# Kernel optimization log

Hardware: AMD Instinct MI355X
Metric: run time of the kernel (lower is better)

## Reference

```python
import jax, jax.numpy as jnp
import numpy as np

N_EDGES = 1_000_000  # also n_atoms (module uses h_s.shape[0] as n_atoms)
N_RADIAL = 8


def setup_inputs() -> dict:
    key = jax.random.key(0)
    k1, k2, k3, k4 = jax.random.split(key, 4)
    dn = jax.random.normal(k1, (N_EDGES, 3), dtype=jnp.float32)
    h_s = jax.random.normal(k2, (N_EDGES, N_RADIAL), dtype=jnp.float32)
    basis = jax.random.uniform(k3, (N_EDGES, N_RADIAL), dtype=jnp.float32)
    idx_i = jax.random.randint(k4, (N_EDGES,), 0, N_EDGES, dtype=jnp.int32)
    return {"dn": dn, "h_s": h_s, "basis": basis, "idx_i": idx_i}


def reference(dn, h_s, basis, idx_i):
    n_atoms = h_s.shape[0]
    # per-edge moments
    zero_moment = h_s * basis                                   # [nbrs, r]
    first_moment = zero_moment[:, :, None] * dn[:, None, :]     # [nbrs, r, 3]
    # scatter-add edges -> atoms
    zero_moment = jax.ops.segment_sum(zero_moment, idx_i, num_segments=n_atoms)   # [a, r]
    first_moment = jax.ops.segment_sum(first_moment, idx_i, num_segments=n_atoms)  # [a, r, 3]
    # contractions over the small radial/spatial dims
    h_s0 = zero_moment                                           # [a, r]
    h_s1 = jnp.einsum('ari,asi->ars', first_moment, first_moment)  # [a, r, r]
    h_s1 = h_s1.reshape(n_atoms, -1)                             # [a, r*r]
    h_p = jnp.einsum('ar,asi->airs', zero_moment, first_moment)  # [a, 3, r, r]
    h_p = h_p.reshape(n_atoms, 3, -1)                            # [a, 3, r*r]
    h_s_out = jnp.concatenate([h_s0, h_s1], axis=-1)             # [a, r + r*r]
    return h_s_out, h_p
```

## Files before the change

kernel.cpp:

```cpp
#include <hip/hip_runtime.h>

#define NR 8
#define SCAN_BS 256
#define SCAN_E  1024
#define FIN_ATOMS 128


__device__ __forceinline__ unsigned short f2b(float f) {
    unsigned int u = __float_as_uint(f);
    unsigned int r = (u + 0x7FFFu + ((u >> 16) & 1u)) >> 16;
    return (unsigned short)r;
}
__device__ __forceinline__ float b2f(unsigned short h) {
    return __uint_as_float(((unsigned int)h) << 16);
}

__global__ void count_kernel(const int* __restrict__ idx,
                             int* __restrict__ cnt,
                             int* __restrict__ rank, int n_edges) {
    int e = blockIdx.x * blockDim.x + threadIdx.x;
    if (e < n_edges) rank[e] = atomicAdd(&cnt[idx[e]], 1);
}

__global__ void scan1_kernel(const int* __restrict__ cnt,
                             int* __restrict__ scanned,
                             int* __restrict__ partial, int n) {
    __shared__ int sh[SCAN_BS];
    int b = blockIdx.x, t = threadIdx.x;
    int base = b * SCAN_E + t * 4;
    int c0 = (base + 0 < n) ? cnt[base + 0] : 0;
    int c1 = (base + 1 < n) ? cnt[base + 1] : 0;
    int c2 = (base + 2 < n) ? cnt[base + 2] : 0;
    int c3 = (base + 3 < n) ? cnt[base + 3] : 0;
    int s = c0 + c1 + c2 + c3;
    sh[t] = s;
    __syncthreads();
    for (int off = 1; off < SCAN_BS; off <<= 1) {
        int v = (t >= off) ? sh[t - off] : 0;
        __syncthreads();
        sh[t] += v;
        __syncthreads();
    }
    int incl = sh[t];
    int excl = incl - s;
    if (base + 0 < n) scanned[base + 0] = excl;
    if (base + 1 < n) scanned[base + 1] = excl + c0;
    if (base + 2 < n) scanned[base + 2] = excl + c0 + c1;
    if (base + 3 < n) scanned[base + 3] = excl + c0 + c1 + c2;
    if (t == SCAN_BS - 1) partial[b] = incl;
}

__global__ void scan2_kernel(int* __restrict__ partial, int nb) {
    __shared__ int sh[1024];
    int t = threadIdx.x;
    int v = (t < nb) ? partial[t] : 0;
    sh[t] = v;
    __syncthreads();
    for (int off = 1; off < 1024; off <<= 1) {
        int u = (t >= off) ? sh[t - off] : 0;
        __syncthreads();
        sh[t] += u;
        __syncthreads();
    }
    if (t < nb) partial[t] = sh[t] - v;
}

__global__ void scan3_kernel(int* __restrict__ offsets,
                             const int* __restrict__ partial,
                             int n, int total) {
    int i = blockIdx.x * blockDim.x + threadIdx.x;
    if (i < n) offsets[i] += partial[i >> 10];
    if (i == 0) offsets[n] = total;
}

__global__ void __launch_bounds__(256) scatter24_kernel(
        const float* __restrict__ dn,
        const float* __restrict__ hs,
        const float* __restrict__ basis,
        const int*   __restrict__ idx,
        const int*   __restrict__ offsets,
        const int*   __restrict__ rank,
        unsigned short* __restrict__ ordered,
        int n_edges) {
    int e = blockIdx.x * blockDim.x + threadIdx.x;
    if (e >= n_edges) return;

    const float4* hsp = reinterpret_cast<const float4*>(hs + (size_t)e * NR);
    const float4* bp  = reinterpret_cast<const float4*>(basis + (size_t)e * NR);
    float4 h0 = hsp[0], h1 = hsp[1];
    float4 b0 = bp[0],  b1 = bp[1];

    float d0 = dn[(size_t)e * 3 + 0];
    float d1 = dn[(size_t)e * 3 + 1];
    float d2 = dn[(size_t)e * 3 + 2];

    unsigned int w0 = (unsigned int)f2b(h0.x * b0.x) | ((unsigned int)f2b(h0.y * b0.y) << 16);
    unsigned int w1 = (unsigned int)f2b(h0.z * b0.z) | ((unsigned int)f2b(h0.w * b0.w) << 16);
    unsigned int w2 = (unsigned int)f2b(h1.x * b1.x) | ((unsigned int)f2b(h1.y * b1.y) << 16);
    unsigned int w3 = (unsigned int)f2b(h1.z * b1.z) | ((unsigned int)f2b(h1.w * b1.w) << 16);
    unsigned int w4 = (unsigned int)f2b(d0) | ((unsigned int)f2b(d1) << 16);
    unsigned int w5 = (unsigned int)f2b(d2);

    int slot = offsets[idx[e]] + rank[e];
    uint2* dst = reinterpret_cast<uint2*>(ordered + (size_t)slot * 12);
    dst[0] = make_uint2(w0, w1);
    dst[1] = make_uint2(w2, w3);
    dst[2] = make_uint2(w4, w5);
}

__global__ void __launch_bounds__(256) contract_fused_kernel(
        const unsigned short* __restrict__ ordered,
        const int* __restrict__ offsets,
        float* __restrict__ out, int n_atoms) {
    __shared__ float sa[FIN_ATOMS][36];
    __shared__ int soff[FIN_ATOMS + 1];

    int a0 = blockIdx.x * FIN_ATOMS;
    int t = threadIdx.x;

    if (t < FIN_ATOMS + 1) {
        int a = a0 + t;
        soff[t] = offsets[(a <= n_atoms) ? a : n_atoms];
    }
    __syncthreads();

    int wave = t >> 6;
    int lane = t & 63;
    int half = lane >> 5;
    int l    = lane & 31;
    int k    = l - 8;
    int s_i  = k & 7;
    int i_i  = k >> 3;
    int src1 = (l < 8) ? l : s_i;
    int src2 = 8 + ((l < 8) ? 0 : i_i);
    bool isz = (l < 8);

#pragma unroll 4
    for (int p = 0; p < FIN_ATOMS / 8; ++p) {
        int al = wave * (FIN_ATOMS / 4) + p * 2 + half;
        int atom = a0 + al;
        if (atom < n_atoms) {
            int start = soff[al];
            int end   = soff[al + 1];
            float x = 0.f;
            for (int b = start; b < end; ++b) {
                const unsigned short* rec = ordered + (size_t)b * 12;
                float v1 = b2f(rec[src1]);
                float v2 = isz ? 1.0f : b2f(rec[src2]);
                x = fmaf(v1, v2, x);
            }
            sa[al][l] = x;
        }
    }
    __syncthreads();

    {
        float4* hs_base = reinterpret_cast<float4*>(out + (size_t)a0 * 72);
        for (int F = t; F < FIN_ATOMS * 18; F += 256) {
            int al = F / 18;
            int kq = F - al * 18;
            if (a0 + al >= n_atoms) break;
            const float* z = sa[al];
            float4 v;
            if (kq < 2) {
                v = reinterpret_cast<const float4*>(z)[kq];
            } else {
                int m = 4 * (kq - 2);
                int r = m >> 3, s = m & 7;
                float  fr0 = z[8 + 0 * 8 + r];
                float  fr1 = z[8 + 1 * 8 + r];
                float  fr2 = z[8 + 2 * 8 + r];
                float4 fs0 = *reinterpret_cast<const float4*>(z + 8 + 0 * 8 + s);
                float4 fs1 = *reinterpret_cast<const float4*>(z + 8 + 1 * 8 + s);
                float4 fs2 = *reinterpret_cast<const float4*>(z + 8 + 2 * 8 + s);
                v.x = fr0 * fs0.x + fr1 * fs1.x + fr2 * fs2.x;
                v.y = fr0 * fs0.y + fr1 * fs1.y + fr2 * fs2.y;
                v.z = fr0 * fs0.z + fr1 * fs1.z + fr2 * fs2.z;
                v.w = fr0 * fs0.w + fr1 * fs1.w + fr2 * fs2.w;
            }
            hs_base[F] = v;
        }
    }
    {
        float4* hp_base = reinterpret_cast<float4*>(
            out + (size_t)n_atoms * 72 + (size_t)a0 * 192);
        for (int F = t; F < FIN_ATOMS * 48; F += 256) {
            int al = F / 48;
            int kq = F - al * 48;
            if (a0 + al >= n_atoms) break;
            const float* z = sa[al];
            int i = kq >> 4;
            int m = (4 * kq) & 63;
            int r = m >> 3, s = m & 7;
            float  zr = z[r];
            float4 fv = *reinterpret_cast<const float4*>(z + 8 + i * 8 + s);
            hp_base[F] = make_float4(zr * fv.x, zr * fv.y, zr * fv.z, zr * fv.w);
        }
    }
}


__global__ void zero_acc_kernel(float* __restrict__ out, int n_atoms) {
    int tid = blockIdx.x * blockDim.x + threadIdx.x;
    if (tid >= n_atoms * 8) return;
    int atom = tid >> 3;
    int q    = tid & 7;
    float4 z = make_float4(0.f, 0.f, 0.f, 0.f);
    if (q < 2) {
        reinterpret_cast<float4*>(out + (size_t)atom * 72)[q] = z;
    } else {
        reinterpret_cast<float4*>(out + (size_t)n_atoms * 72 + (size_t)atom * 192)[q - 2] = z;
    }
}

__global__ void scatter_atomic_kernel(const float* __restrict__ dn,
                                      const float* __restrict__ hs,
                                      const float* __restrict__ basis,
                                      const int*   __restrict__ idx,
                                      float* __restrict__ out,
                                      int n_edges, int n_atoms) {
    int e = blockIdx.x * blockDim.x + threadIdx.x;
    if (e >= n_edges) return;

    const float4* hsp = reinterpret_cast<const float4*>(hs + (size_t)e * NR);
    const float4* bp  = reinterpret_cast<const float4*>(basis + (size_t)e * NR);
    float4 h0 = hsp[0], h1 = hsp[1];
    float4 b0 = bp[0],  b1 = bp[1];

    float d0 = dn[(size_t)e * 3 + 0];
    float d1 = dn[(size_t)e * 3 + 1];
    float d2 = dn[(size_t)e * 3 + 2];

    float zm[NR];
    zm[0] = h0.x * b0.x; zm[1] = h0.y * b0.y; zm[2] = h0.z * b0.z; zm[3] = h0.w * b0.w;
    zm[4] = h1.x * b1.x; zm[5] = h1.y * b1.y; zm[6] = h1.z * b1.z; zm[7] = h1.w * b1.w;

    int a = idx[e];
    float* zp = out + (size_t)a * 72;
    float* fp = out + (size_t)n_atoms * 72 + (size_t)a * 192;

#pragma unroll
    for (int r = 0; r < NR; ++r) atomicAdd(zp + r, zm[r]);
#pragma unroll
    for (int r = 0; r < NR; ++r) {
        atomicAdd(fp + r * 3 + 0, zm[r] * d0);
        atomicAdd(fp + r * 3 + 1, zm[r] * d1);
        atomicAdd(fp + r * 3 + 2, zm[r] * d2);
    }
}

__global__ void contract_inplace_kernel(float* __restrict__ out, int n_atoms) {
    int atom = blockIdx.x * 4 + (threadIdx.x >> 6);
    if (atom >= n_atoms) return;
    int lane = threadIdx.x & 63;

    float* zrow = out + (size_t)atom * 72;
    float* prow = out + (size_t)n_atoms * 72 + (size_t)atom * 192;

    float x = 0.f;
    if (lane < 8)       x = zrow[lane];
    else if (lane < 32) x = prow[lane - 8];

    int r = lane >> 3;
    int s = lane & 7;

    float zr  = __shfl(x, r);
    float fr0 = __shfl(x, 8 + r * 3 + 0);
    float fr1 = __shfl(x, 8 + r * 3 + 1);
    float fr2 = __shfl(x, 8 + r * 3 + 2);
    float fs0 = __shfl(x, 8 + s * 3 + 0);
    float fs1 = __shfl(x, 8 + s * 3 + 1);
    float fs2 = __shfl(x, 8 + s * 3 + 2);

    float hs1 = fr0 * fs0 + fr1 * fs1 + fr2 * fs2;

    zrow[8 + lane] = hs1;
    prow[lane]       = zr * fs0;
    prow[64 + lane]  = zr * fs1;
    prow[128 + lane] = zr * fs2;
}


extern "C" void kernel_launch(void* const* d_in, const int* in_sizes, int n_in,
                              void* d_out, int out_size, void* d_ws, size_t ws_size,
                              hipStream_t stream) {
    const float* dn    = (const float*)d_in[0];
    const float* hs    = (const float*)d_in[1];
    const float* basis = (const float*)d_in[2];
    const int*   idx   = (const int*)d_in[3];
    float* out = (float*)d_out;

    int n_edges = in_sizes[0] / 3;
    int n_atoms = in_sizes[1] / NR;
    int nb1 = (n_atoms + SCAN_E - 1) / SCAN_E;

    size_t off_offs = (size_t)n_atoms * 4;
    size_t off_rank = off_offs + (size_t)(n_atoms + 1) * 4;
    size_t off_part = off_rank + (size_t)n_edges * 4;
    size_t off_ord  = (off_part + (size_t)nb1 * 4 + 255) & ~(size_t)255;
    size_t ws_needed = off_ord + (size_t)n_edges * 24;

    if (ws_size >= ws_needed && nb1 <= 1024) {
        char* ws = (char*)d_ws;
        int* cnt     = (int*)ws;
        int* offsets = (int*)(ws + off_offs);
        int* rank    = (int*)(ws + off_rank);
        int* partial = (int*)(ws + off_part);
        unsigned short* ordered = (unsigned short*)(ws + off_ord);

        hipMemsetAsync(cnt, 0, (size_t)n_atoms * 4, stream);

        int blk = 256;
        count_kernel<<<(n_edges + blk - 1) / blk, blk, 0, stream>>>(
            idx, cnt, rank, n_edges);

        scan1_kernel<<<nb1, SCAN_BS, 0, stream>>>(cnt, offsets, partial, n_atoms);
        scan2_kernel<<<1, 1024, 0, stream>>>(partial, nb1);
        scan3_kernel<<<(n_atoms + blk - 1) / blk, blk, 0, stream>>>(
            offsets, partial, n_atoms, n_edges);

        scatter24_kernel<<<(n_edges + blk - 1) / blk, blk, 0, stream>>>(
            dn, hs, basis, idx, offsets, rank, ordered, n_edges);

        contract_fused_kernel<<<(n_atoms + FIN_ATOMS - 1) / FIN_ATOMS, 256, 0, stream>>>(
            ordered, offsets, out, n_atoms);
    } else {
        int blk = 256;
        int total = n_atoms * 8;
        zero_acc_kernel<<<(total + blk - 1) / blk, blk, 0, stream>>>(out, n_atoms);
        scatter_atomic_kernel<<<(n_edges + blk - 1) / blk, blk, 0, stream>>>(
            dn, hs, basis, idx, out, n_edges, n_atoms);
        contract_inplace_kernel<<<(n_atoms + 3) / 4, 256, 0, stream>>>(out, n_atoms);
    }
}
```

Measured before the change: 346.8 us.

## Bucket edges by 128-atom block and accumulate with LDS atomics

Replaces the per-atom counting sort (per-atom counts, three-stage scan, per-edge rank) with a coarse sort into 128-atom buckets. Bucket counts are scanned in a single block, and edges are scattered through atomic cursors, with the local atom index packed into the spare 16 bits of each record. The contract kernel streams each bucket's records coalesced and accumulates the 32 moment values per edge with shared-memory float atomics. This removes the rank array, two scan launches and the serial per-atom loops, at the cost of 32 LDS atomics per edge and a nondeterministic summation order.

```diff
diff --git a/kernel.cpp b/kernel.cpp
--- a/kernel.cpp
+++ b/kernel.cpp
@@ -1,9 +1,8 @@
 #include <hip/hip_runtime.h>
 
 #define NR 8
-#define SCAN_BS 256
-#define SCAN_E  1024
 #define FIN_ATOMS 128
+#define MAX_NB 8192
 
 
 __device__ __forceinline__ unsigned short f2b(float f) {
@@ -15,71 +14,57 @@
     return __uint_as_float(((unsigned int)h) << 16);
 }
 
-__global__ void count_kernel(const int* __restrict__ idx,
-                             int* __restrict__ cnt,
-                             int* __restrict__ rank, int n_edges) {
+__global__ void count_bucket_kernel(const int* __restrict__ idx,
+                                    int* __restrict__ cnt, int n_edges) {
     int e = blockIdx.x * blockDim.x + threadIdx.x;
-    if (e < n_edges) rank[e] = atomicAdd(&cnt[idx[e]], 1);
-}
-
-__global__ void scan1_kernel(const int* __restrict__ cnt,
-                             int* __restrict__ scanned,
-                             int* __restrict__ partial, int n) {
-    __shared__ int sh[SCAN_BS];
-    int b = blockIdx.x, t = threadIdx.x;
-    int base = b * SCAN_E + t * 4;
-    int c0 = (base + 0 < n) ? cnt[base + 0] : 0;
-    int c1 = (base + 1 < n) ? cnt[base + 1] : 0;
-    int c2 = (base + 2 < n) ? cnt[base + 2] : 0;
-    int c3 = (base + 3 < n) ? cnt[base + 3] : 0;
-    int s = c0 + c1 + c2 + c3;
+    if (e < n_edges) atomicAdd(&cnt[idx[e] >> 7], 1);
+}
+
+__global__ void __launch_bounds__(1024) scan_bucket_kernel(
+        const int* __restrict__ cnt,
+        int* __restrict__ boff,
+        int* __restrict__ cursor,
+        int nb, int total) {
+    __shared__ int sh[1024];
+    int t = threadIdx.x;
+    int per = (nb + 1023) >> 10;
+    int base = t * per;
+    int loc[8];
+    int s = 0;
+#pragma unroll 8
+    for (int k = 0; k < 8; ++k) {
+        if (k < per) {
+            int v = (base + k < nb) ? cnt[base + k] : 0;
+            loc[k] = s;
+            s += v;
+        }
+    }
     sh[t] = s;
     __syncthreads();
-    for (int off = 1; off < SCAN_BS; off <<= 1) {
+    for (int off = 1; off < 1024; off <<= 1) {
         int v = (t >= off) ? sh[t - off] : 0;
         __syncthreads();
         sh[t] += v;
         __syncthreads();
     }
-    int incl = sh[t];
-    int excl = incl - s;
-    if (base + 0 < n) scanned[base + 0] = excl;
-    if (base + 1 < n) scanned[base + 1] = excl + c0;
-    if (base + 2 < n) scanned[base + 2] = excl + c0 + c1;
-    if (base + 3 < n) scanned[base + 3] = excl + c0 + c1 + c2;
-    if (t == SCAN_BS - 1) partial[b] = incl;
-}
-
-__global__ void scan2_kernel(int* __restrict__ partial, int nb) {
-    __shared__ int sh[1024];
-    int t = threadIdx.x;
-    int v = (t < nb) ? partial[t] : 0;
-    sh[t] = v;
-    __syncthreads();
-    for (int off = 1; off < 1024; off <<= 1) {
-        int u = (t >= off) ? sh[t - off] : 0;
-        __syncthreads();
-        sh[t] += u;
-        __syncthreads();
-    }
-    if (t < nb) partial[t] = sh[t] - v;
-}
-
-__global__ void scan3_kernel(int* __restrict__ offsets,
-                             const int* __restrict__ partial,
-                             int n, int total) {
-    int i = blockIdx.x * blockDim.x + threadIdx.x;
-    if (i < n) offsets[i] += partial[i >> 10];
-    if (i == 0) offsets[n] = total;
-}
-
-__global__ void __launch_bounds__(256) scatter24_kernel(
+    int excl = sh[t] - s;
+#pragma unroll 8
+    for (int k = 0; k < 8; ++k) {
+        if (k < per && base + k < nb) {
+            int o = excl + loc[k];
+            boff[base + k]   = o;
+            cursor[base + k] = o;
+        }
+    }
+    if (t == 0) boff[nb] = total;
+}
+
+__global__ void __launch_bounds__(256) scatter_bucket_kernel(
         const float* __restrict__ dn,
         const float* __restrict__ hs,
         const float* __restrict__ basis,
         const int*   __restrict__ idx,
-        const int*   __restrict__ offsets,
-        const int*   __restrict__ rank,
+        int*         __restrict__ cursor,
         unsigned short* __restrict__ ordered,
         int n_edges) {
     int e = blockIdx.x * blockDim.x + threadIdx.x;
@@ -93,64 +78,69 @@
     float d0 = dn[(size_t)e * 3 + 0];
     float d1 = dn[(size_t)e * 3 + 1];
     float d2 = dn[(size_t)e * 3 + 2];
+
+    int a  = idx[e];
+    int b  = a >> 7;
+    unsigned int al = (unsigned int)(a & (FIN_ATOMS - 1));
 
     unsigned int w0 = (unsigned int)f2b(h0.x * b0.x) | ((unsigned int)f2b(h0.y * b0.y) << 16);
     unsigned int w1 = (unsigned int)f2b(h0.z * b0.z) | ((unsigned int)f2b(h0.w * b0.w) << 16);
     unsigned int w2 = (unsigned int)f2b(h1.x * b1.x) | ((unsigned int)f2b(h1.y * b1.y) << 16);
     unsigned int w3 = (unsigned int)f2b(h1.z * b1.z) | ((unsigned int)f2b(h1.w * b1.w) << 16);
     unsigned int w4 = (unsigned int)f2b(d0) | ((unsigned int)f2b(d1) << 16);
-    unsigned int w5 = (unsigned int)f2b(d2);
-
-    int slot = offsets[idx[e]] + rank[e];
+    unsigned int w5 = (unsigned int)f2b(d2) | (al << 16);
+
+    int slot = atomicAdd(&cursor[b], 1);
     uint2* dst = reinterpret_cast<uint2*>(ordered + (size_t)slot * 12);
     dst[0] = make_uint2(w0, w1);
     dst[1] = make_uint2(w2, w3);
     dst[2] = make_uint2(w4, w5);
 }
 
-__global__ void __launch_bounds__(256) contract_fused_kernel(
+__global__ void __launch_bounds__(256) contract_bucket_kernel(
         const unsigned short* __restrict__ ordered,
-        const int* __restrict__ offsets,
+        const int* __restrict__ boff,
         float* __restrict__ out, int n_atoms) {
     __shared__ float sa[FIN_ATOMS][36];
-    __shared__ int soff[FIN_ATOMS + 1];
-
-    int a0 = blockIdx.x * FIN_ATOMS;
-    int t = threadIdx.x;
-
-    if (t < FIN_ATOMS + 1) {
-        int a = a0 + t;
-        soff[t] = offsets[(a <= n_atoms) ? a : n_atoms];
-    }
+
+    int bi = blockIdx.x;
+    int a0 = bi * FIN_ATOMS;
+    int t  = threadIdx.x;
+
+    float* flat = &sa[0][0];
+    for (int i = t; i < FIN_ATOMS * 36; i += 256) flat[i] = 0.f;
     __syncthreads();
 
-    int wave = t >> 6;
-    int lane = t & 63;
-    int half = lane >> 5;
-    int l    = lane & 31;
-    int k    = l - 8;
-    int s_i  = k & 7;
-    int i_i  = k >> 3;
-    int src1 = (l < 8) ? l : s_i;
-    int src2 = 8 + ((l < 8) ? 0 : i_i);
-    bool isz = (l < 8);
-
-#pragma unroll 4
-    for (int p = 0; p < FIN_ATOMS / 8; ++p) {
-        int al = wave * (FIN_ATOMS / 4) + p * 2 + half;
-        int atom = a0 + al;
-        if (atom < n_atoms) {
-            int start = soff[al];
-            int end   = soff[al + 1];
-            float x = 0.f;
-            for (int b = start; b < end; ++b) {
-                const unsigned short* rec = ordered + (size_t)b * 12;
-                float v1 = b2f(rec[src1]);
-                float v2 = isz ? 1.0f : b2f(rec[src2]);
-                x = fmaf(v1, v2, x);
-            }
-            sa[al][l] = x;
-        }
+    int j0 = boff[bi];
+    int j1 = boff[bi + 1];
+
+    for (int j = j0 + t; j < j1; j += 256) {
+        const uint2* rp = reinterpret_cast<const uint2*>(ordered + (size_t)j * 12);
+        uint2 q0 = rp[0], q1 = rp[1], q2 = rp[2];
+
+        float zm[8];
+        zm[0] = b2f((unsigned short)(q0.x & 0xFFFF));
+        zm[1] = b2f((unsigned short)(q0.x >> 16));
+        zm[2] = b2f((unsigned short)(q0.y & 0xFFFF));
+        zm[3] = b2f((unsigned short)(q0.y >> 16));
+        zm[4] = b2f((unsigned short)(q1.x & 0xFFFF));
+        zm[5] = b2f((unsigned short)(q1.x >> 16));
+        zm[6] = b2f((unsigned short)(q1.y & 0xFFFF));
+        zm[7] = b2f((unsigned short)(q1.y >> 16));
+        float d0 = b2f((unsigned short)(q2.x & 0xFFFF));
+        float d1 = b2f((unsigned short)(q2.x >> 16));
+        float d2 = b2f((unsigned short)(q2.y & 0xFFFF));
+        int   al = (int)(q2.y >> 16);
+
+        float* acc = sa[al];
+#pragma unroll
+        for (int s = 0; s < 8; ++s) atomicAdd(&acc[s], zm[s]);
+#pragma unroll
+        for (int s = 0; s < 8; ++s) atomicAdd(&acc[8 + s],  zm[s] * d0);
+#pragma unroll
+        for (int s = 0; s < 8; ++s) atomicAdd(&acc[16 + s], zm[s] * d1);
+#pragma unroll
+        for (int s = 0; s < 8; ++s) atomicAdd(&acc[24 + s], zm[s] * d2);
     }
     __syncthreads();
 
@@ -292,38 +282,33 @@
 
     int n_edges = in_sizes[0] / 3;
     int n_atoms = in_sizes[1] / NR;
-    int nb1 = (n_atoms + SCAN_E - 1) / SCAN_E;
-
-    size_t off_offs = (size_t)n_atoms * 4;
-    size_t off_rank = off_offs + (size_t)(n_atoms + 1) * 4;
-    size_t off_part = off_rank + (size_t)n_edges * 4;
-    size_t off_ord  = (off_part + (size_t)nb1 * 4 + 255) & ~(size_t)255;
+    int nb = (n_atoms + FIN_ATOMS - 1) / FIN_ATOMS;
+
+    size_t off_boff = (size_t)nb * 4;
+    size_t off_cur  = off_boff + (size_t)(nb + 1) * 4;
+    size_t off_ord  = (off_cur + (size_t)nb * 4 + 255) & ~(size_t)255;
     size_t ws_needed = off_ord + (size_t)n_edges * 24;
 
-    if (ws_size >= ws_needed && nb1 <= 1024) {
+    if (ws_size >= ws_needed && nb <= MAX_NB) {
         char* ws = (char*)d_ws;
-        int* cnt     = (int*)ws;
-        int* offsets = (int*)(ws + off_offs);
-        int* rank    = (int*)(ws + off_rank);
-        int* partial = (int*)(ws + off_part);
+        int* cnt    = (int*)ws;
+        int* boff   = (int*)(ws + off_boff);
+        int* cursor = (int*)(ws + off_cur);
         unsigned short* ordered = (unsigned short*)(ws + off_ord);
 
-        hipMemsetAsync(cnt, 0, (size_t)n_atoms * 4, stream);
+        (void)hipMemsetAsync(cnt, 0, (size_t)nb * 4, stream);
 
         int blk = 256;
-        count_kernel<<<(n_edges + blk - 1) / blk, blk, 0, stream>>>(
-            idx, cnt, rank, n_edges);
-
-        scan1_kernel<<<nb1, SCAN_BS, 0, stream>>>(cnt, offsets, partial, n_atoms);
-        scan2_kernel<<<1, 1024, 0, stream>>>(partial, nb1);
-        scan3_kernel<<<(n_atoms + blk - 1) / blk, blk, 0, stream>>>(
-            offsets, partial, n_atoms, n_edges);
-
-        scatter24_kernel<<<(n_edges + blk - 1) / blk, blk, 0, stream>>>(
-            dn, hs, basis, idx, offsets, rank, ordered, n_edges);
-
-        contract_fused_kernel<<<(n_atoms + FIN_ATOMS - 1) / FIN_ATOMS, 256, 0, stream>>>(
-            ordered, offsets, out, n_atoms);
+        count_bucket_kernel<<<(n_edges + blk - 1) / blk, blk, 0, stream>>>(
+            idx, cnt, n_edges);
+
+        scan_bucket_kernel<<<1, 1024, 0, stream>>>(cnt, boff, cursor, nb, n_edges);
+
+        scatter_bucket_kernel<<<(n_edges + blk - 1) / blk, blk, 0, stream>>>(
+            dn, hs, basis, idx, cursor, ordered, n_edges);
+
+        contract_bucket_kernel<<<nb, 256, 0, stream>>>(
+            ordered, boff, out, n_atoms);
     } else {
         int blk = 256;
         int total = n_atoms * 8;
```

New measurement: 345.2 us. Within noise of the previous version (-0.5%).
